# Optimization experiments

Hardware: AMD Instinct MI355X
Metric: run time of the kernel (lower is better)

Reference implementation:

```python
import jax, jax.numpy as jnp
import numpy as np

SHAPE0 = (256, 256)   # top pyramid level (h, w)
SIGMA = 3.0
EPS = 1e-3
BATCH = 128
N_CHAN = 3
N_LEVELS = 4
N_PIX = sum((SHAPE0[0] >> i) * (SHAPE0[1] >> i) for i in range(N_LEVELS))  # 87040


def _gauss_lum_kernel(sigma):
    # 2D Gaussian times RGB luminance weights -> HWIO kernel (kh, kw, 3, 1)
    s = int(np.ceil(2 * sigma))
    u = np.linspace(-s, s, 2 * s + 1)
    g = np.exp(-(u[:, None] ** 2 + u[None, :] ** 2) / (2 * sigma ** 2)) / (2 * np.pi * sigma ** 2)
    w = np.array([0.2989, 0.587, 0.114])
    k = (g[:, :, None, None] * w[None, None, :, None]).astype(np.float32)
    return jnp.asarray(k)


def _conv_same(x, k):
    # NHWC conv with zero 'SAME' padding; equivalent to the original
    # pad(s) + SAME conv + center crop (net effect is SAME with zero pad).
    return jax.lax.conv_general_dilated(
        x, k, window_strides=(1, 1), padding='SAME',
        dimension_numbers=('NHWC', 'HWIO', 'NHWC'))


def setup_inputs() -> dict:
    key = jax.random.key(0)
    x = jax.random.uniform(key, (BATCH, N_PIX, N_CHAN), dtype=jnp.float32)
    return {"x": x}


def reference(x):
    k = _gauss_lum_kernel(SIGMA)
    n_pix, nc = x.shape[1], x.shape[2]
    h, w = SHAPE0
    outs = []
    i = 0
    while i + h * w <= n_pix:  # static Python loop over pyramid levels
        xi = x[:, i:i + h * w, :].reshape(-1, h, w, nc)          # (B,h,w,3)
        lum = _conv_same(xi, k)                                   # (B,h,w,1)
        dens = _conv_same(jnp.ones((1, h, w, nc), x.dtype), k)    # (1,h,w,1), input-independent
        outs.append((xi / (lum / dens + EPS)).reshape(-1, h * w, nc))
        i += h * w
        h //= 2
        w //= 2
    return jnp.concatenate(outs, axis=1)  # packed pyramid (B, n_pix, 3)
```

## Files before the change

kernel.cpp:

```cpp
#include <hip/hip_runtime.h>


#define NPIX   87040
#define EPSV   1e-3f
#define WSUM   0.9999f
#define TW     64
#define TH     16
#define RAD    6
#define LW     80
#define LWP    84
#define RCP    68
#define LH     28
#define NPXH   (LH * LW)
#define NBLK   11008
#define NXCD   8
#define CHUNK  (NBLK / NXCD)

__device__ __constant__ float G1[13] = {
    0.01799699f, 0.03315904f, 0.05467002f, 0.08065689f, 0.10648267f,
    0.12579441f, 0.13298076f, 0.12579441f, 0.10648267f, 0.08065689f,
    0.05467002f, 0.03315904f, 0.01799699f
};
__device__ __constant__ float PRE[14] = {
    0.00000000f, 0.01799699f, 0.05115603f, 0.10582605f, 0.18648294f,
    0.29296561f, 0.41876002f, 0.55174078f, 0.67753519f, 0.78401786f,
    0.86467475f, 0.91934477f, 0.95250381f, 0.97050080f
};

struct F3 { float x, y, z; };

__global__ __launch_bounds__(256)
void mslln_kernel(const float* __restrict__ x, float* __restrict__ out) {
    __shared__ float s_mem[LH * LWP];
    __shared__ float s_rc[LH][RCP];
    float (*s_lum)[LWP]   = (float(*)[LWP])s_mem;
    float (*s_scale)[RCP] = (float(*)[RCP])s_mem;

    const int bphys = blockIdx.x;
    const int bid   = (bphys & (NXCD - 1)) * CHUNK + (bphys >> 3);
    const int t     = threadIdx.x;

    int img, tl, txlog, h, off;
    if (bid < 8192)       { img = bid >> 6;                 tl = bid & 63; txlog = 2; h = 256; off = 0;     }
    else if (bid < 10240) { int r = bid - 8192;  img = r >> 4; tl = r & 15; txlog = 1; h = 128; off = 65536; }
    else if (bid < 10752) { int r = bid - 10240; img = r >> 2; tl = r & 3;  txlog = 0; h = 64;  off = 81920; }
    else                  { int r = bid - 10752; img = r >> 1; tl = r & 1;  txlog = 0; h = 32;  off = 86016; }
    const int w   = h;
    const int tx0 = (tl & ((1 << txlog) - 1)) << 6;
    const int ty0 = (tl >> txlog) << 4;

    const float* __restrict__ xb = x   + (size_t)img * (NPIX * 3) + (size_t)off * 3;
    float*       __restrict__ ob = out + (size_t)img * (NPIX * 3) + (size_t)off * 3;

#pragma unroll
    for (int k = 0; k < 9; k++) {
        int i = t + (k << 8);
        if (i < NPXH) {
            int r  = i / LW;
            int c  = i - r * LW;
            int gy = ty0 + r - RAD;
            int gx = tx0 + c - 8;
            float lum = 0.f;
            if (gy >= 0 && gy < h && gx >= 0 && gx < w) {
                F3 v = *(const F3*)(xb + ((size_t)gy * w + gx) * 3);
                lum = 0.2989f * v.x + 0.587f * v.y + 0.114f * v.z;
            }
            s_lum[r][c] = lum;
        }
    }
    __syncthreads();

    F3 pf[4];
#pragma unroll
    for (int j = 0; j < 4; j++) {
        int P   = t + (j << 8);
        int row = P >> 6, col = P & 63;
        int gx  = tx0 + col;
        pf[j].x = 0.f; pf[j].y = 0.f; pf[j].z = 0.f;
        if (gx < w)
            pf[j] = *(const F3*)(xb + ((size_t)(ty0 + row) * w + gx) * 3);
    }

#pragma unroll
    for (int k = 0; k < 2; k++) {
        int gi = t + (k << 8);
        if (gi < 448) {
            int r  = gi >> 4;
            int c4 = (gi & 15) << 2;
            float a[20];
#pragma unroll
            for (int m = 0; m < 5; m++)
                *(float4*)&a[m << 2] = *(const float4*)&s_lum[r][c4 + (m << 2)];
            float s0 = 0.f, s1 = 0.f, s2 = 0.f, s3 = 0.f;
#pragma unroll
            for (int j = 0; j < 13; j++) {
                float gj = G1[j];
                s0 += a[2 + j] * gj;
                s1 += a[3 + j] * gj;
                s2 += a[4 + j] * gj;
                s3 += a[5 + j] * gj;
            }
            *(float4*)&s_rc[r][c4] = make_float4(s0, s1, s2, s3);
        }
    }
    __syncthreads();

    {
        int ly  = t >> 4;
        int lx4 = (t & 15) << 2;
        if (tx0 + lx4 < w) {
            float4 acc = {0.f, 0.f, 0.f, 0.f};
#pragma unroll
            for (int j = 0; j < 13; j++) {
                float4 v = *(const float4*)&s_rc[ly + j][lx4];
                float gj = G1[j];
                acc.x += v.x * gj; acc.y += v.y * gj;
                acc.z += v.z * gj; acc.w += v.w * gj;
            }
            int gy = ty0 + ly;
            int ylo = min(RAD, gy), yhi = min(RAD, h - 1 - gy);
            float Sy = PRE[RAD + yhi + 1] - PRE[RAD - ylo];
            float4 sc;
#pragma unroll
            for (int d = 0; d < 4; d++) {
                int gx = tx0 + lx4 + d;
                int xlo = min(RAD, gx), xhi = min(RAD, w - 1 - gx);
                float Sx = PRE[RAD + xhi + 1] - PRE[RAD - xlo];
                float dens = WSUM * Sy * Sx;
                float s = (d == 0) ? acc.x : (d == 1) ? acc.y : (d == 2) ? acc.z : acc.w;
                float r = dens / (s + EPSV * dens);
                if (d == 0) sc.x = r; else if (d == 1) sc.y = r;
                else if (d == 2) sc.z = r; else sc.w = r;
            }
            *(float4*)&s_scale[ly][lx4] = sc;
        }
    }
    __syncthreads();

#pragma unroll
    for (int j = 0; j < 4; j++) {
        int P   = t + (j << 8);
        int row = P >> 6, col = P & 63;
        int gx  = tx0 + col;
        if (gx < w) {
            float sc = s_scale[row][col];
            F3 v = pf[j];
            v.x *= sc; v.y *= sc; v.z *= sc;
            *(F3*)(ob + ((size_t)(ty0 + row) * w + gx) * 3) = v;
        }
    }
}

extern "C" void kernel_launch(void* const* d_in, const int* in_sizes, int n_in,
                              void* d_out, int out_size, void* d_ws, size_t ws_size,
                              hipStream_t stream) {
    const float* x = (const float*)d_in[0];
    float* out = (float*)d_out;
    mslln_kernel<<<NBLK, 256, 0, stream>>>(x, out);
}
```

Before: 254.4 us.

## Process two tiles per block with software-prefetched halo loads

Each block now handles two consecutive tiles, issuing global loads of the next tile's halo into registers while the current tile's separable convolution runs, which aims to hide memory latency. Halo index math is precomputed once per thread, and the center-pixel loads are re-indexed to row strides. This halves the grid size and raises register pressure from the 9-entry raw buffer, which may reduce occupancy and adds an extra barrier per tile.

```diff
diff --git a/kernel.cpp b/kernel.cpp
--- a/kernel.cpp
+++ b/kernel.cpp
@@ -4,17 +4,16 @@
 #define NPIX   87040
 #define EPSV   1e-3f
 #define WSUM   0.9999f
-#define TW     64
-#define TH     16
 #define RAD    6
 #define LW     80
 #define LWP    84
 #define RCP    68
 #define LH     28
 #define NPXH   (LH * LW)
-#define NBLK   11008
+#define NT     2
+#define NPAIR  (11008 / NT)
 #define NXCD   8
-#define CHUNK  (NBLK / NXCD)
+#define CHUNK  (NPAIR / NXCD)
 
 __device__ __constant__ float G1[13] = {
     0.01799699f, 0.03315904f, 0.05467002f, 0.08065689f, 0.10648267f,
@@ -29,6 +28,20 @@
 
 struct F3 { float x, y, z; };
 
+__device__ __forceinline__ void decode_tile(int bid, const float* x, float* out,
+    const float*& xb, float*& ob, int& w, int& h, int& tx0, int& ty0) {
+    int img, tl, txlog, off;
+    if (bid < 8192)       { img = bid >> 6;                 tl = bid & 63; txlog = 2; h = 256; off = 0;     }
+    else if (bid < 10240) { int r = bid - 8192;  img = r >> 4; tl = r & 15; txlog = 1; h = 128; off = 65536; }
+    else if (bid < 10752) { int r = bid - 10240; img = r >> 2; tl = r & 3;  txlog = 0; h = 64;  off = 81920; }
+    else                  { int r = bid - 10752; img = r >> 1; tl = r & 1;  txlog = 0; h = 32;  off = 86016; }
+    w   = h;
+    tx0 = (tl & ((1 << txlog) - 1)) << 6;
+    ty0 = (tl >> txlog) << 4;
+    xb  = x   + (size_t)img * (NPIX * 3) + (size_t)off * 3;
+    ob  = out + (size_t)img * (NPIX * 3) + (size_t)off * 3;
+}
+
 __global__ __launch_bounds__(256)
 void mslln_kernel(const float* __restrict__ x, float* __restrict__ out) {
     __shared__ float s_mem[LH * LWP];
@@ -37,116 +50,146 @@
     float (*s_scale)[RCP] = (float(*)[RCP])s_mem;
 
     const int bphys = blockIdx.x;
-    const int bid   = (bphys & (NXCD - 1)) * CHUNK + (bphys >> 3);
+    const int pair  = (bphys & (NXCD - 1)) * CHUNK + (bphys >> 3);
     const int t     = threadIdx.x;
 
-    int img, tl, txlog, h, off;
-    if (bid < 8192)       { img = bid >> 6;                 tl = bid & 63; txlog = 2; h = 256; off = 0;     }
-    else if (bid < 10240) { int r = bid - 8192;  img = r >> 4; tl = r & 15; txlog = 1; h = 128; off = 65536; }
-    else if (bid < 10752) { int r = bid - 10240; img = r >> 2; tl = r & 3;  txlog = 0; h = 64;  off = 81920; }
-    else                  { int r = bid - 10752; img = r >> 1; tl = r & 1;  txlog = 0; h = 32;  off = 86016; }
-    const int w   = h;
-    const int tx0 = (tl & ((1 << txlog) - 1)) << 6;
-    const int ty0 = (tl >> txlog) << 4;
-
-    const float* __restrict__ xb = x   + (size_t)img * (NPIX * 3) + (size_t)off * 3;
-    float*       __restrict__ ob = out + (size_t)img * (NPIX * 3) + (size_t)off * 3;
-
+    int hrc[9];
 #pragma unroll
     for (int k = 0; k < 9; k++) {
         int i = t + (k << 8);
-        if (i < NPXH) {
-            int r  = i / LW;
-            int c  = i - r * LW;
-            int gy = ty0 + r - RAD;
-            int gx = tx0 + c - 8;
-            float lum = 0.f;
-            if (gy >= 0 && gy < h && gx >= 0 && gx < w) {
-                F3 v = *(const F3*)(xb + ((size_t)gy * w + gx) * 3);
-                lum = 0.2989f * v.x + 0.587f * v.y + 0.114f * v.z;
-            }
-            s_lum[r][c] = lum;
-        }
+        int r = i / LW;
+        hrc[k] = (r << 7) | (i - r * LW);
+    }
+    const bool h8   = (t < NPXH - 8 * 256);
+    const int  prow = t >> 6;
+    const int  pcol = t & 63;
+
+    const float* xb; float* ob; int w, h, tx0, ty0;
+    decode_tile(pair * NT, x, out, xb, ob, w, h, tx0, ty0);
+
+    F3 raw[9];
+#pragma unroll
+    for (int k = 0; k < 9; k++) {
+        raw[k].x = 0.f; raw[k].y = 0.f; raw[k].z = 0.f;
+        if (k < 8 || h8) {
+            int gy = ty0 + (hrc[k] >> 7) - RAD;
+            int gx = tx0 + (hrc[k] & 127) - 8;
+            if (gy >= 0 && gy < h && gx >= 0 && gx < w)
+                raw[k] = *(const F3*)(xb + ((size_t)gy * w + gx) * 3);
+        }
+    }
+#pragma unroll
+    for (int k = 0; k < 9; k++)
+        if (k < 8 || h8)
+            s_lum[hrc[k] >> 7][hrc[k] & 127] =
+                0.2989f * raw[k].x + 0.587f * raw[k].y + 0.114f * raw[k].z;
+
+    F3 pf[4];
+#pragma unroll
+    for (int j = 0; j < 4; j++) {
+        pf[j].x = 0.f; pf[j].y = 0.f; pf[j].z = 0.f;
+        if (tx0 + pcol < w)
+            pf[j] = *(const F3*)(xb + ((size_t)(ty0 + prow + 4 * j) * w + tx0 + pcol) * 3);
     }
     __syncthreads();
 
-    F3 pf[4];
-#pragma unroll
-    for (int j = 0; j < 4; j++) {
-        int P   = t + (j << 8);
-        int row = P >> 6, col = P & 63;
-        int gx  = tx0 + col;
-        pf[j].x = 0.f; pf[j].y = 0.f; pf[j].z = 0.f;
-        if (gx < w)
-            pf[j] = *(const F3*)(xb + ((size_t)(ty0 + row) * w + gx) * 3);
-    }
-
-#pragma unroll
-    for (int k = 0; k < 2; k++) {
-        int gi = t + (k << 8);
-        if (gi < 448) {
-            int r  = gi >> 4;
-            int c4 = (gi & 15) << 2;
-            float a[20];
-#pragma unroll
-            for (int m = 0; m < 5; m++)
-                *(float4*)&a[m << 2] = *(const float4*)&s_lum[r][c4 + (m << 2)];
-            float s0 = 0.f, s1 = 0.f, s2 = 0.f, s3 = 0.f;
-#pragma unroll
-            for (int j = 0; j < 13; j++) {
-                float gj = G1[j];
-                s0 += a[2 + j] * gj;
-                s1 += a[3 + j] * gj;
-                s2 += a[4 + j] * gj;
-                s3 += a[5 + j] * gj;
-            }
-            *(float4*)&s_rc[r][c4] = make_float4(s0, s1, s2, s3);
-        }
-    }
-    __syncthreads();
-
-    {
-        int ly  = t >> 4;
-        int lx4 = (t & 15) << 2;
-        if (tx0 + lx4 < w) {
-            float4 acc = {0.f, 0.f, 0.f, 0.f};
-#pragma unroll
-            for (int j = 0; j < 13; j++) {
-                float4 v = *(const float4*)&s_rc[ly + j][lx4];
-                float gj = G1[j];
-                acc.x += v.x * gj; acc.y += v.y * gj;
-                acc.z += v.z * gj; acc.w += v.w * gj;
-            }
-            int gy = ty0 + ly;
-            int ylo = min(RAD, gy), yhi = min(RAD, h - 1 - gy);
-            float Sy = PRE[RAD + yhi + 1] - PRE[RAD - ylo];
-            float4 sc;
-#pragma unroll
-            for (int d = 0; d < 4; d++) {
-                int gx = tx0 + lx4 + d;
-                int xlo = min(RAD, gx), xhi = min(RAD, w - 1 - gx);
-                float Sx = PRE[RAD + xhi + 1] - PRE[RAD - xlo];
-                float dens = WSUM * Sy * Sx;
-                float s = (d == 0) ? acc.x : (d == 1) ? acc.y : (d == 2) ? acc.z : acc.w;
-                float r = dens / (s + EPSV * dens);
-                if (d == 0) sc.x = r; else if (d == 1) sc.y = r;
-                else if (d == 2) sc.z = r; else sc.w = r;
-            }
-            *(float4*)&s_scale[ly][lx4] = sc;
-        }
-    }
-    __syncthreads();
-
-#pragma unroll
-    for (int j = 0; j < 4; j++) {
-        int P   = t + (j << 8);
-        int row = P >> 6, col = P & 63;
-        int gx  = tx0 + col;
-        if (gx < w) {
-            float sc = s_scale[row][col];
-            F3 v = pf[j];
-            v.x *= sc; v.y *= sc; v.z *= sc;
-            *(F3*)(ob + ((size_t)(ty0 + row) * w + gx) * 3) = v;
+    const float* xbn; float* obn; int wn, hn, txn, tyn;
+#pragma unroll
+    for (int tt = 0; tt < NT; tt++) {
+        if (tt + 1 < NT) {
+            decode_tile(pair * NT + tt + 1, x, out, xbn, obn, wn, hn, txn, tyn);
+#pragma unroll
+            for (int k = 0; k < 9; k++) {
+                raw[k].x = 0.f; raw[k].y = 0.f; raw[k].z = 0.f;
+                if (k < 8 || h8) {
+                    int gy = tyn + (hrc[k] >> 7) - RAD;
+                    int gx = txn + (hrc[k] & 127) - 8;
+                    if (gy >= 0 && gy < hn && gx >= 0 && gx < wn)
+                        raw[k] = *(const F3*)(xbn + ((size_t)gy * wn + gx) * 3);
+                }
+            }
+        }
+
+#pragma unroll
+        for (int k2 = 0; k2 < 2; k2++) {
+            int gi = t + (k2 << 8);
+            if (gi < 448) {
+                int r  = gi >> 4;
+                int c4 = (gi & 15) << 2;
+                float a[20];
+#pragma unroll
+                for (int m = 0; m < 5; m++)
+                    *(float4*)&a[m << 2] = *(const float4*)&s_lum[r][c4 + (m << 2)];
+                float s0 = 0.f, s1 = 0.f, s2 = 0.f, s3 = 0.f;
+#pragma unroll
+                for (int j = 0; j < 13; j++) {
+                    float gj = G1[j];
+                    s0 += a[2 + j] * gj;
+                    s1 += a[3 + j] * gj;
+                    s2 += a[4 + j] * gj;
+                    s3 += a[5 + j] * gj;
+                }
+                *(float4*)&s_rc[r][c4] = make_float4(s0, s1, s2, s3);
+            }
+        }
+        __syncthreads();
+
+        {
+            int ly = t >> 4, lx4 = (t & 15) << 2;
+            if (tx0 + lx4 < w) {
+                float4 acc = {0.f, 0.f, 0.f, 0.f};
+#pragma unroll
+                for (int j = 0; j < 13; j++) {
+                    float4 v = *(const float4*)&s_rc[ly + j][lx4];
+                    float gj = G1[j];
+                    acc.x += v.x * gj; acc.y += v.y * gj;
+                    acc.z += v.z * gj; acc.w += v.w * gj;
+                }
+                int gy = ty0 + ly;
+                int ylo = min(RAD, gy), yhi = min(RAD, h - 1 - gy);
+                float Sy = PRE[RAD + yhi + 1] - PRE[RAD - ylo];
+                float4 sc;
+#pragma unroll
+                for (int d = 0; d < 4; d++) {
+                    int gx = tx0 + lx4 + d;
+                    int xlo = min(RAD, gx), xhi = min(RAD, w - 1 - gx);
+                    float Sx = PRE[RAD + xhi + 1] - PRE[RAD - xlo];
+                    float dens = WSUM * Sy * Sx;
+                    float s = (d == 0) ? acc.x : (d == 1) ? acc.y : (d == 2) ? acc.z : acc.w;
+                    float r = dens / (s + EPSV * dens);
+                    if (d == 0) sc.x = r; else if (d == 1) sc.y = r;
+                    else if (d == 2) sc.z = r; else sc.w = r;
+                }
+                *(float4*)&s_scale[ly][lx4] = sc;
+            }
+        }
+        __syncthreads();
+
+        if (tx0 + pcol < w) {
+#pragma unroll
+            for (int j = 0; j < 4; j++) {
+                float sc = s_scale[prow + 4 * j][pcol];
+                F3 v = pf[j];
+                v.x *= sc; v.y *= sc; v.z *= sc;
+                *(F3*)(ob + ((size_t)(ty0 + prow + 4 * j) * w + tx0 + pcol) * 3) = v;
+            }
+        }
+
+        if (tt + 1 < NT) {
+            __syncthreads();
+#pragma unroll
+            for (int k = 0; k < 9; k++)
+                if (k < 8 || h8)
+                    s_lum[hrc[k] >> 7][hrc[k] & 127] =
+                        0.2989f * raw[k].x + 0.587f * raw[k].y + 0.114f * raw[k].z;
+#pragma unroll
+            for (int j = 0; j < 4; j++) {
+                pf[j].x = 0.f; pf[j].y = 0.f; pf[j].z = 0.f;
+                if (txn + pcol < wn)
+                    pf[j] = *(const F3*)(xbn + ((size_t)(tyn + prow + 4 * j) * wn + txn + pcol) * 3);
+            }
+            xb = xbn; ob = obn; w = wn; h = hn; tx0 = txn; ty0 = tyn;
+            __syncthreads();
         }
     }
 }
@@ -156,5 +199,5 @@
                               hipStream_t stream) {
     const float* x = (const float*)d_in[0];
     float* out = (float*)d_out;
-    mslln_kernel<<<NBLK, 256, 0, stream>>>(x, out);
+    mslln_kernel<<<NPAIR, 256, 0, stream>>>(x, out);
 }
```

Measured after the change: 281.5 us. 1.11x slower.
